# Kernel tuning notes

Hardware: AMD Instinct MI355X
Metric: run time of the kernel (lower is better)

## Reference

```python
import jax, jax.numpy as jnp
import numpy as np

HEADS = 4
KNN = 32
N_KEYS = 512
K_DIM = 512
HALF = K_DIM // 2
V_DIM = 1024
IN_DIM = 1024


def setup_inputs() -> dict:
    key = jax.random.key(0)
    k1, k2, k3, k4, k5 = jax.random.split(key, 5)
    x = jax.random.normal(k1, (1, 2048, IN_DIM), dtype=jnp.float32)
    w_q = jax.random.normal(k2, (HEADS * K_DIM, IN_DIM), dtype=jnp.float32) * (IN_DIM ** -0.5)
    b_q = jax.random.normal(k3, (HEADS * K_DIM,), dtype=jnp.float32) * 0.01
    # subkeys: uniform(-1/sqrt(half), 1/sqrt(half)) as in get_uniform_keys
    bound = 1.0 / np.sqrt(HALF)
    keys = jax.random.uniform(k4, (HEADS, 2, N_KEYS, HALF), dtype=jnp.float32,
                              minval=-bound, maxval=bound)
    # values: normal(0, v_dim**-0.5)
    values = jax.random.normal(k5, (N_KEYS * N_KEYS, V_DIM), dtype=jnp.float32) * (V_DIM ** -0.5)
    return {"x": x, "w_q": w_q, "b_q": b_q, "keys": keys, "values": values}


def reference(x, w_q, b_q, keys, values):
    B, S, D = x.shape
    bs = B * S
    # query projection: (bs, heads*k_dim) -> (bs, heads, 2, half)
    q = (x.reshape(bs, D) @ w_q.T + b_q).reshape(bs, HEADS, 2, HALF)
    # per-head, per-half subkey scores: (bs, heads, 2, n_keys)
    scores = jnp.einsum('bhtd,htnd->bhtn', q, keys)
    s_top, i_top = jax.lax.top_k(scores, KNN)          # (bs, heads, 2, knn)
    s1, s2 = s_top[:, :, 0], s_top[:, :, 1]
    i1, i2 = i_top[:, :, 0], i_top[:, :, 1]
    # cross-product of the two half top-k sets: (bs, heads, knn*knn)
    all_s = (s1[..., :, None] + s2[..., None, :]).reshape(bs, HEADS, KNN * KNN)
    all_i = (i1[..., :, None] * N_KEYS + i2[..., None, :]).reshape(bs, HEADS, KNN * KNN)
    best_s, best_pos = jax.lax.top_k(all_s, KNN)       # (bs, heads, knn)
    idx = jnp.take_along_axis(all_i, best_pos, axis=-1)
    # softmax over knn per head (matches softmax on scores.view(-1, knn))
    w = jax.nn.softmax(best_s, axis=-1).reshape(bs, HEADS * KNN)
    idx = idx.reshape(bs, HEADS * KNN)
    # weighted EmbeddingBag gather-sum over the value table
    out = jnp.einsum('bk,bkd->bd', w, values[idx])     # (bs, v_dim)
    return out.reshape(B, S, V_DIM)
```

## Files before the change

### kernel.cpp

```cpp
#include <hip/hip_runtime.h>
#include <math.h>

#define BSZ   2048
#define INDIM 1024
#define QDIM  2048
#define NHT   8
#define NKEYS 512
#define HALFD 256
#define KNN   32
#define VDIM  1024
#define HEADS 4

typedef _Float16 v8h __attribute__((ext_vector_type(8)));
typedef _Float16 v4h __attribute__((ext_vector_type(4)));
typedef float    v4f __attribute__((ext_vector_type(4)));

template<int KSHIFT, bool ASIDE>
__device__ __forceinline__ void split4(const float* __restrict__ in,
                                       _Float16* __restrict__ out, int i) {
  const long e0 = (long)i * 4;
  const int K = 1 << KSHIFT;
  const long r = e0 >> KSHIFT;
  const int k = (int)(e0 & (K - 1));
  const float4 a = *(const float4*)&in[e0];
  const float av[4] = {a.x, a.y, a.z, a.w};
  v4h hv, dv, mv;
  #pragma unroll
  for (int u = 0; u < 4; ++u) {
    const _Float16 hh = (_Float16)av[u];
    hv[u] = hh;
    mv[u] = (_Float16)((av[u] - (float)hh) * 64.0f);
    dv[u] = (_Float16)((float)hh * 0.015625f);
  }
  _Float16* base = out + r * (3L * K) + k;
  *(v4h*)(base)         = hv;
  *(v4h*)(base + K)     = ASIDE ? dv : mv;
  *(v4h*)(base + 2 * K) = ASIDE ? mv : dv;
}

__global__ __launch_bounds__(256) void split_all_kernel(
    const float* __restrict__ x, const float* __restrict__ wq, const float* __restrict__ ky,
    _Float16* __restrict__ xs, _Float16* __restrict__ wqs, _Float16* __restrict__ kys) {
  const int i = blockIdx.x * 256 + threadIdx.x;
  if (i < 524288)            split4<10, true >(x,  xs,  i);
  else if (i < 1048576)      split4<10, false>(wq, wqs, i - 524288);
  else                       split4<8,  false>(ky, kys, i - 1048576);
}

__device__ __forceinline__ void gload16(const _Float16* g, _Float16* l) {
  __builtin_amdgcn_global_load_lds(
      (const __attribute__((address_space(1))) unsigned int*)g,
      (__attribute__((address_space(3))) unsigned int*)l, 16, 0, 0);
}

#define WAITV8 asm volatile("s_waitcnt vmcnt(8)" ::: "memory")
#define WAITV4 asm volatile("s_waitcnt vmcnt(4)" ::: "memory")
#define WAITV0 asm volatile("s_waitcnt vmcnt(0)" ::: "memory")

template<bool Q_EPI>
__global__ __launch_bounds__(256) void mfma_gemm(
    const _Float16* __restrict__ A, int lda, long aBS,
    const _Float16* __restrict__ B, int ldb, long bBS,
    const float* __restrict__ bias,
    float* __restrict__ Cf, int ldc, long cBS,
    _Float16* __restrict__ Cq, int K) {
  __shared__ __align__(16) char smem[65536];
  _Float16* sh = (_Float16*)smem;
  const int t = threadIdx.x;
  const int z = blockIdx.z;
  const _Float16* Ab = A + (size_t)z * aBS;
  const _Float16* Bb = B + (size_t)z * bBS;
  const int m0 = blockIdx.y * 128, n0 = blockIdx.x * 128;

  const int o0 = t * 16;
  const int os = o0 ^ (((o0 >> 7) & 3) << 4);
  const int sr = os >> 6;
  const int sk = (os & 63) >> 1;
  const _Float16* gA0 = Ab + (size_t)(m0 + sr) * lda + sk;
  const _Float16* gA1 = Ab + (size_t)(m0 + sr + 64) * lda + sk;
  const _Float16* gB0 = Bb + (size_t)(n0 + sr) * ldb + sk;
  const _Float16* gB1 = Bb + (size_t)(n0 + sr + 64) * ldb + sk;
  const int t8 = t * 8;

  const int lane = t & 63, w = t >> 6;
  const int wr = (w >> 1) * 64, wc = (w & 1) * 64;
  const int fr = lane & 15, kg = lane >> 4;

  int aoff[4], boff[4];
  #pragma unroll
  for (int i = 0; i < 4; ++i) {
    const int ra = wr + i * 16 + fr;
    aoff[i] = (ra * 64 + ((kg ^ ((ra >> 1) & 3)) * 16)) >> 1;
    const int rb = wc + i * 16 + fr;
    boff[i] = ((rb * 64 + ((kg ^ ((rb >> 1) & 3)) * 16)) >> 1) + 4096;
  }

  v4f acc[4][4];
  #pragma unroll
  for (int i = 0; i < 4; ++i)
    #pragma unroll
    for (int j = 0; j < 4; ++j)
      acc[i][j] = (v4f){0.f, 0.f, 0.f, 0.f};

  const int nt = K >> 5;

  #pragma unroll
  for (int p = 0; p < 3; ++p) {
    _Float16* bb = sh + p * 8192;
    const size_t ko = (size_t)p * 32;
    gload16(gA0 + ko, bb + t8);
    gload16(gA1 + ko, bb + 2048 + t8);
    gload16(gB0 + ko, bb + 4096 + t8);
    gload16(gB1 + ko, bb + 6144 + t8);
  }
  WAITV8;
  __builtin_amdgcn_s_barrier();
  __builtin_amdgcn_sched_barrier(0);

  for (int tt = 0; tt < nt; ++tt) {
    const _Float16* bb = sh + (tt & 3) * 8192;
    if (tt + 3 < nt) {
      _Float16* nb = sh + ((tt + 3) & 3) * 8192;
      const size_t ko = (size_t)(tt + 3) * 32;
      gload16(gA0 + ko, nb + t8);
      gload16(gA1 + ko, nb + 2048 + t8);
      gload16(gB0 + ko, nb + 4096 + t8);
      gload16(gB1 + ko, nb + 6144 + t8);
    }
    v8h af[4], bf[4];
    #pragma unroll
    for (int i = 0; i < 4; ++i) af[i] = *(const v8h*)(bb + aoff[i]);
    #pragma unroll
    for (int j = 0; j < 4; ++j) bf[j] = *(const v8h*)(bb + boff[j]);
    #pragma unroll
    for (int i = 0; i < 4; ++i)
      #pragma unroll
      for (int j = 0; j < 4; ++j)
        acc[i][j] = __builtin_amdgcn_mfma_f32_16x16x32_f16(af[i], bf[j], acc[i][j], 0, 0, 0);
    if (tt + 3 < nt)      { WAITV8; }
    else if (tt + 2 < nt) { WAITV4; }
    else if (tt + 1 < nt) { WAITV0; }
    __builtin_amdgcn_s_barrier();
    __builtin_amdgcn_sched_barrier(0);
  }

  if (Q_EPI) {
    float* Ct = (float*)smem;
    #pragma unroll
    for (int half = 0; half < 2; ++half) {
      __syncthreads();
      if ((w & 1) == half) {
        #pragma unroll
        for (int j = 0; j < 4; ++j) {
          const int colq = j * 16 + fr;
          const float bv = bias[n0 + half * 64 + colq];
          #pragma unroll
          for (int i = 0; i < 4; ++i)
            #pragma unroll
            for (int rr = 0; rr < 4; ++rr)
              Ct[(wr + i * 16 + kg * 4 + rr) * 68 + colq] = acc[i][j][rr] + bv;
        }
      }
      __syncthreads();
      const int r = t >> 1, cb = (t & 1) * 32;
      const int gcol = n0 + half * 64 + cb;
      const int ht = gcol >> 8, dd = gcol & 255;
      _Float16* p = Cq + (size_t)(m0 + r) * (3 * HALFD * NHT) + ht * (3 * HALFD) + dd;
      #pragma unroll
      for (int u = 0; u < 32; u += 8) {
        float vv[8];
        *(float4*)&vv[0] = *(const float4*)&Ct[r * 68 + cb + u];
        *(float4*)&vv[4] = *(const float4*)&Ct[r * 68 + cb + u + 4];
        v8h hv, dv, mv;
        #pragma unroll
        for (int e = 0; e < 8; ++e) {
          const _Float16 hh = (_Float16)vv[e];
          hv[e] = hh;
          mv[e] = (_Float16)((vv[e] - (float)hh) * 64.0f);
          dv[e] = (_Float16)((float)hh * 0.015625f);
        }
        *(v8h*)(p + u) = hv;
        *(v8h*)(p + HALFD + u) = dv;
        *(v8h*)(p + 2 * HALFD + u) = mv;
      }
    }
  } else {
    float* Cb = Cf + (size_t)z * cBS;
    #pragma unroll
    for (int i = 0; i < 4; ++i)
      #pragma unroll
      for (int j = 0; j < 4; ++j)
        #pragma unroll
        for (int rr = 0; rr < 4; ++rr) {
          const int rowg = m0 + wr + i * 16 + kg * 4 + rr;
          const int colg = n0 + wc + j * 16 + fr;
          Cb[(size_t)rowg * ldc + colg] = acc[i][j][rr];
        }
  }
}

__global__ __launch_bounds__(256) void topk_all_gather_kernel(
    const float* __restrict__ S, const float* __restrict__ values,
    float* __restrict__ out) {
  __shared__ float ls1[4][32], ls2[4][32], sels[4][32];
  __shared__ int   li1[4][32], li2[4][32], seli[4][32];
  __shared__ float lw[128];
  __shared__ int   lidx[128];
  const int b = blockIdx.x, t = threadIdx.x;
  const int lane = t & 63, h = t >> 6;
  const float* srA = S + ((size_t)b * NHT + 2 * h) * NKEYS;
  const float* srB = srA + NKEYS;
  float va[8], vb[8];
  #pragma unroll
  for (int j = 0; j < 8; ++j) va[j] = srA[j * 64 + lane];
  #pragma unroll
  for (int j = 0; j < 8; ++j) vb[j] = srB[j * 64 + lane];

  for (int r = 0; r < KNN; ++r) {
    float bv = -INFINITY; int bi = 0x7fffffff;
    #pragma unroll
    for (int j = 0; j < 8; ++j) {
      const int idx = j * 64 + lane;
      if (va[j] > bv) { bv = va[j]; bi = idx; }
    }
    #pragma unroll
    for (int off = 32; off > 0; off >>= 1) {
      const float ov = __shfl_xor(bv, off);
      const int oi = __shfl_xor(bi, off);
      if (ov > bv || (ov == bv && oi < bi)) { bv = ov; bi = oi; }
    }
    if (lane == 0) { ls1[h][r] = bv; li1[h][r] = bi; }
    const int jj = bi >> 6;
    const bool mine = (bi & 63) == lane;
    #pragma unroll
    for (int j = 0; j < 8; ++j)
      if (mine && j == jj) va[j] = -INFINITY;
  }
  for (int r = 0; r < KNN; ++r) {
    float bv = -INFINITY; int bi = 0x7fffffff;
    #pragma unroll
    for (int j = 0; j < 8; ++j) {
      const int idx = j * 64 + lane;
      if (vb[j] > bv) { bv = vb[j]; bi = idx; }
    }
    #pragma unroll
    for (int off = 32; off > 0; off >>= 1) {
      const float ov = __shfl_xor(bv, off);
      const int oi = __shfl_xor(bi, off);
      if (ov > bv || (ov == bv && oi < bi)) { bv = ov; bi = oi; }
    }
    if (lane == 0) { ls2[h][r] = bv; li2[h][r] = bi; }
    const int jj = bi >> 6;
    const bool mine = (bi & 63) == lane;
    #pragma unroll
    for (int j = 0; j < 8; ++j)
      if (mine && j == jj) vb[j] = -INFINITY;
  }

  float v[16];
  #pragma unroll
  for (int c = 0; c < 16; ++c) {
    const int p = c * 64 + lane;
    v[c] = ls1[h][p >> 5] + ls2[h][p & 31];
  }
  for (int r = 0; r < KNN; ++r) {
    float bv = -INFINITY; int bp = 0x7fffffff;
    #pragma unroll
    for (int c = 0; c < 16; ++c) {
      const int p = c * 64 + lane;
      if (v[c] > bv) { bv = v[c]; bp = p; }
    }
    #pragma unroll
    for (int off = 32; off > 0; off >>= 1) {
      const float ov = __shfl_xor(bv, off);
      const int op = __shfl_xor(bp, off);
      if (ov > bv || (ov == bv && op < bp)) { bv = ov; bp = op; }
    }
    if (lane == 0) {
      sels[h][r] = bv;
      seli[h][r] = li1[h][bp >> 5] * NKEYS + li2[h][bp & 31];
    }
    const int cc = bp >> 6;
    const bool mine = (bp & 63) == lane;
    #pragma unroll
    for (int c = 0; c < 16; ++c)
      if (mine && c == cc) v[c] = -INFINITY;
  }
  const float m = sels[h][0];
  const float e = (lane < 32) ? expf(sels[h][lane] - m) : 0.0f;
  float s = e;
  #pragma unroll
  for (int off = 32; off > 0; off >>= 1) s += __shfl_xor(s, off);
  if (lane < 32) {
    lw[h * 32 + lane] = e / s;
    lidx[h * 32 + lane] = seli[h][lane];
  }
  __syncthreads();
  const int d0 = t * 4;
  float4 acc = {0.f, 0.f, 0.f, 0.f};
  #pragma unroll 8
  for (int k = 0; k < 128; ++k) {
    const float4 vv = *(const float4*)&values[(size_t)lidx[k] * VDIM + d0];
    const float ww = lw[k];
    acc.x = fmaf(ww, vv.x, acc.x);
    acc.y = fmaf(ww, vv.y, acc.y);
    acc.z = fmaf(ww, vv.z, acc.z);
    acc.w = fmaf(ww, vv.w, acc.w);
  }
  *(float4*)&out[(size_t)b * VDIM + d0] = acc;
}

extern "C" void kernel_launch(void* const* d_in, const int* in_sizes, int n_in,
                              void* d_out, int out_size, void* d_ws, size_t ws_size,
                              hipStream_t stream) {
  const float* x      = (const float*)d_in[0];
  const float* w_q    = (const float*)d_in[1];
  const float* b_q    = (const float*)d_in[2];
  const float* keys   = (const float*)d_in[3];
  const float* values = (const float*)d_in[4];
  float* out = (float*)d_out;

  char* ws = (char*)d_ws;
  _Float16* xs    = (_Float16*)(ws);
  _Float16* wqs   = (_Float16*)(ws + (16u  << 20));
  _Float16* keyss = (_Float16*)(ws + (32u  << 20));
  _Float16* Qs    = (_Float16*)(ws + (40u  << 20));
  float*    S     = (float*)   (ws + (68u  << 20));

  split_all_kernel<<<5120, 256, 0, stream>>>(x, w_q, keys, xs, wqs, keyss);

  mfma_gemm<true><<<dim3(QDIM / 128, BSZ / 128, 1), 256, 0, stream>>>(
      xs, 3 * INDIM, 0, wqs, 3 * INDIM, 0, b_q,
      nullptr, 0, 0, Qs, 3 * INDIM);
  mfma_gemm<false><<<dim3(NKEYS / 128, BSZ / 128, NHT), 256, 0, stream>>>(
      Qs, 3 * HALFD * NHT, 3 * HALFD, keyss, 3 * HALFD, (long)NKEYS * 3 * HALFD, nullptr,
      S, NHT * NKEYS, NKEYS, nullptr, 3 * HALFD);

  topk_all_gather_kernel<<<BSZ, 256, 0, stream>>>(S, values, out);
}
```

Baseline: 333.7 us.

## Deepen GEMM1 K-tile and overlap value gathers with top-k selection

The first projection GEMM becomes a dedicated kernel with a 64-wide K tile, a 4-stage LDS ring using 128KB of shared memory, and an 8-way XOR swizzle. Fewer, larger loop iterations are meant to cut barrier and issue overhead. The top-k/gather kernel now fetches each selected value row right after it is chosen and accumulates an online-softmax weighted sum per head, with a one-step software prefetch. A shared-memory reduction across the four heads replaces the separate 128-row gather loop, hiding gather latency behind selection. The cost is higher LDS use per block in GEMM1, which limits occupancy, and a changed floating-point summation order.

```diff
diff --git a/kernel.cpp b/kernel.cpp
--- a/kernel.cpp
+++ b/kernel.cpp
@@ -53,17 +53,145 @@
       (__attribute__((address_space(3))) unsigned int*)l, 16, 0, 0);
 }
 
-#define WAITV8 asm volatile("s_waitcnt vmcnt(8)" ::: "memory")
-#define WAITV4 asm volatile("s_waitcnt vmcnt(4)" ::: "memory")
-#define WAITV0 asm volatile("s_waitcnt vmcnt(0)" ::: "memory")
-
-template<bool Q_EPI>
-__global__ __launch_bounds__(256) void mfma_gemm(
+#define WAITV16 asm volatile("s_waitcnt vmcnt(16)" ::: "memory")
+#define WAITV8  asm volatile("s_waitcnt vmcnt(8)" ::: "memory")
+#define WAITV4  asm volatile("s_waitcnt vmcnt(4)" ::: "memory")
+#define WAITV0  asm volatile("s_waitcnt vmcnt(0)" ::: "memory")
+
+__global__ __launch_bounds__(256) void gemm1_kernel(
+    const _Float16* __restrict__ A, const _Float16* __restrict__ B,
+    const float* __restrict__ bias, _Float16* __restrict__ Cq) {
+  __shared__ __align__(16) char smem[131072];
+  _Float16* sh = (_Float16*)smem;
+  const int t = threadIdx.x;
+  const int m0 = blockIdx.y * 128, n0 = blockIdx.x * 128;
+  const int lane = t & 63, w = t >> 6;
+  const int wr = (w >> 1) * 64, wc = (w & 1) * 64;
+  const int fr = lane & 15, kg = lane >> 4;
+
+  const _Float16* gA[4]; const _Float16* gB[4];
+  int dA[4], dB[4];
+  #pragma unroll
+  for (int p = 0; p < 4; ++p) {
+    const int O = p * 4096 + t * 16;
+    const int os = O ^ (((O >> 7) & 7) << 4);
+    const int srow = os >> 7, sk = (os & 127) >> 1;
+    gA[p] = A + (size_t)(m0 + srow) * 3072 + sk;
+    gB[p] = B + (size_t)(n0 + srow) * 3072 + sk;
+    dA[p] = O >> 1;
+    dB[p] = (16384 + O) >> 1;
+  }
+
+  int aof[2][4], bof[2][4];
+  #pragma unroll
+  for (int ks = 0; ks < 2; ++ks)
+    #pragma unroll
+    for (int i = 0; i < 4; ++i) {
+      const int ra = wr + i * 16 + fr;
+      aof[ks][i] = (ra * 128 + ((((ks << 2) | kg) ^ (fr & 7)) << 4)) >> 1;
+      const int rb = wc + i * 16 + fr;
+      bof[ks][i] = ((rb * 128 + ((((ks << 2) | kg) ^ (fr & 7)) << 4)) >> 1) + 8192;
+    }
+
+  v4f acc[4][4];
+  #pragma unroll
+  for (int i = 0; i < 4; ++i)
+    #pragma unroll
+    for (int j = 0; j < 4; ++j)
+      acc[i][j] = (v4f){0.f, 0.f, 0.f, 0.f};
+
+  const int nt = 48;
+
+  #pragma unroll
+  for (int p2 = 0; p2 < 3; ++p2) {
+    _Float16* bb = sh + p2 * 16384;
+    const size_t ko = (size_t)p2 * 64;
+    #pragma unroll
+    for (int p = 0; p < 4; ++p) {
+      gload16(gA[p] + ko, bb + dA[p]);
+      gload16(gB[p] + ko, bb + dB[p]);
+    }
+  }
+  WAITV16;
+  __builtin_amdgcn_s_barrier();
+  __builtin_amdgcn_sched_barrier(0);
+
+  for (int tt = 0; tt < nt; ++tt) {
+    const _Float16* bb = sh + (tt & 3) * 16384;
+    if (tt + 3 < nt) {
+      _Float16* nb = sh + ((tt + 3) & 3) * 16384;
+      const size_t ko = (size_t)(tt + 3) * 64;
+      #pragma unroll
+      for (int p = 0; p < 4; ++p) {
+        gload16(gA[p] + ko, nb + dA[p]);
+        gload16(gB[p] + ko, nb + dB[p]);
+      }
+    }
+    #pragma unroll
+    for (int ks = 0; ks < 2; ++ks) {
+      v8h af[4], bf[4];
+      #pragma unroll
+      for (int i = 0; i < 4; ++i) af[i] = *(const v8h*)(bb + aof[ks][i]);
+      #pragma unroll
+      for (int j = 0; j < 4; ++j) bf[j] = *(const v8h*)(bb + bof[ks][j]);
+      #pragma unroll
+      for (int i = 0; i < 4; ++i)
+        #pragma unroll
+        for (int j = 0; j < 4; ++j)
+          acc[i][j] = __builtin_amdgcn_mfma_f32_16x16x32_f16(af[i], bf[j], acc[i][j], 0, 0, 0);
+    }
+    if (tt + 3 < nt)      { WAITV16; }
+    else if (tt + 2 < nt) { WAITV8; }
+    else if (tt + 1 < nt) { WAITV0; }
+    __builtin_amdgcn_s_barrier();
+    __builtin_amdgcn_sched_barrier(0);
+  }
+
+  float* Ct = (float*)smem;
+  #pragma unroll
+  for (int half = 0; half < 2; ++half) {
+    __syncthreads();
+    if ((w & 1) == half) {
+      #pragma unroll
+      for (int j = 0; j < 4; ++j) {
+        const int colq = j * 16 + fr;
+        const float bv = bias[n0 + half * 64 + colq];
+        #pragma unroll
+        for (int i = 0; i < 4; ++i)
+          #pragma unroll
+          for (int rr = 0; rr < 4; ++rr)
+            Ct[(wr + i * 16 + kg * 4 + rr) * 68 + colq] = acc[i][j][rr] + bv;
+      }
+    }
+    __syncthreads();
+    const int r = t >> 1, cb = (t & 1) * 32;
+    const int gcol = n0 + half * 64 + cb;
+    const int ht = gcol >> 8, dd = gcol & 255;
+    _Float16* p = Cq + (size_t)(m0 + r) * (3 * HALFD * NHT) + ht * (3 * HALFD) + dd;
+    #pragma unroll
+    for (int u = 0; u < 32; u += 8) {
+      float vv[8];
+      *(float4*)&vv[0] = *(const float4*)&Ct[r * 68 + cb + u];
+      *(float4*)&vv[4] = *(const float4*)&Ct[r * 68 + cb + u + 4];
+      v8h hv, dv, mv;
+      #pragma unroll
+      for (int e = 0; e < 8; ++e) {
+        const _Float16 hh = (_Float16)vv[e];
+        hv[e] = hh;
+        mv[e] = (_Float16)((vv[e] - (float)hh) * 64.0f);
+        dv[e] = (_Float16)((float)hh * 0.015625f);
+      }
+      *(v8h*)(p + u) = hv;
+      *(v8h*)(p + HALFD + u) = dv;
+      *(v8h*)(p + 2 * HALFD + u) = mv;
+    }
+  }
+}
+
+__global__ __launch_bounds__(256) void gemm2_kernel(
     const _Float16* __restrict__ A, int lda, long aBS,
     const _Float16* __restrict__ B, int ldb, long bBS,
-    const float* __restrict__ bias,
-    float* __restrict__ Cf, int ldc, long cBS,
-    _Float16* __restrict__ Cq, int K) {
+    float* __restrict__ Cf, int ldc, long cBS, int K) {
   __shared__ __align__(16) char smem[65536];
   _Float16* sh = (_Float16*)smem;
   const int t = threadIdx.x;
@@ -144,68 +272,25 @@
     __builtin_amdgcn_sched_barrier(0);
   }
 
-  if (Q_EPI) {
-    float* Ct = (float*)smem;
-    #pragma unroll
-    for (int half = 0; half < 2; ++half) {
-      __syncthreads();
-      if ((w & 1) == half) {
-        #pragma unroll
-        for (int j = 0; j < 4; ++j) {
-          const int colq = j * 16 + fr;
-          const float bv = bias[n0 + half * 64 + colq];
-          #pragma unroll
-          for (int i = 0; i < 4; ++i)
-            #pragma unroll
-            for (int rr = 0; rr < 4; ++rr)
-              Ct[(wr + i * 16 + kg * 4 + rr) * 68 + colq] = acc[i][j][rr] + bv;
-        }
+  float* Cb = Cf + (size_t)z * cBS;
+  #pragma unroll
+  for (int i = 0; i < 4; ++i)
+    #pragma unroll
+    for (int j = 0; j < 4; ++j)
+      #pragma unroll
+      for (int rr = 0; rr < 4; ++rr) {
+        const int rowg = m0 + wr + i * 16 + kg * 4 + rr;
+        const int colg = n0 + wc + j * 16 + fr;
+        Cb[(size_t)rowg * ldc + colg] = acc[i][j][rr];
       }
-      __syncthreads();
-      const int r = t >> 1, cb = (t & 1) * 32;
-      const int gcol = n0 + half * 64 + cb;
-      const int ht = gcol >> 8, dd = gcol & 255;
-      _Float16* p = Cq + (size_t)(m0 + r) * (3 * HALFD * NHT) + ht * (3 * HALFD) + dd;
-      #pragma unroll
-      for (int u = 0; u < 32; u += 8) {
-        float vv[8];
-        *(float4*)&vv[0] = *(const float4*)&Ct[r * 68 + cb + u];
-        *(float4*)&vv[4] = *(const float4*)&Ct[r * 68 + cb + u + 4];
-        v8h hv, dv, mv;
-        #pragma unroll
-        for (int e = 0; e < 8; ++e) {
-          const _Float16 hh = (_Float16)vv[e];
-          hv[e] = hh;
-          mv[e] = (_Float16)((vv[e] - (float)hh) * 64.0f);
-          dv[e] = (_Float16)((float)hh * 0.015625f);
-        }
-        *(v8h*)(p + u) = hv;
-        *(v8h*)(p + HALFD + u) = dv;
-        *(v8h*)(p + 2 * HALFD + u) = mv;
-      }
-    }
-  } else {
-    float* Cb = Cf + (size_t)z * cBS;
-    #pragma unroll
-    for (int i = 0; i < 4; ++i)
-      #pragma unroll
-      for (int j = 0; j < 4; ++j)
-        #pragma unroll
-        for (int rr = 0; rr < 4; ++rr) {
-          const int rowg = m0 + wr + i * 16 + kg * 4 + rr;
-          const int colg = n0 + wc + j * 16 + fr;
-          Cb[(size_t)rowg * ldc + colg] = acc[i][j][rr];
-        }
-  }
 }
 
 __global__ __launch_bounds__(256) void topk_all_gather_kernel(
     const float* __restrict__ S, const float* __restrict__ values,
     float* __restrict__ out) {
-  __shared__ float ls1[4][32], ls2[4][32], sels[4][32];
-  __shared__ int   li1[4][32], li2[4][32], seli[4][32];
-  __shared__ float lw[128];
-  __shared__ int   lidx[128];
+  __shared__ float ls1[4][32], ls2[4][32];
+  __shared__ int   li1[4][32], li2[4][32];
+  __shared__ float red[4][1024];
   const int b = blockIdx.x, t = threadIdx.x;
   const int lane = t & 63, h = t >> 6;
   const float* srA = S + ((size_t)b * NHT + 2 * h) * NKEYS;
@@ -263,6 +348,9 @@
     const int p = c * 64 + lane;
     v[c] = ls1[h][p >> 5] + ls2[h][p & 31];
   }
+  float4 acc0 = {0,0,0,0}, acc1 = {0,0,0,0}, acc2 = {0,0,0,0}, acc3 = {0,0,0,0};
+  float4 pv0, pv1, pv2, pv3;
+  float pe = 0.0f, m = 0.0f, Z = 0.0f;
   for (int r = 0; r < KNN; ++r) {
     float bv = -INFINITY; int bp = 0x7fffffff;
     #pragma unroll
@@ -276,38 +364,56 @@
       const int op = __shfl_xor(bp, off);
       if (ov > bv || (ov == bv && op < bp)) { bv = ov; bp = op; }
     }
-    if (lane == 0) {
-      sels[h][r] = bv;
-      seli[h][r] = li1[h][bp >> 5] * NKEYS + li2[h][bp & 31];
-    }
+    const int row = li1[h][bp >> 5] * NKEYS + li2[h][bp & 31];
+    if (r == 0) m = bv;
+    const float e = expf(bv - m);
+    Z += e;
+    const float4* vp = (const float4*)(values + (size_t)row * VDIM) + lane;
+    const float4 c0 = vp[0], c1 = vp[64], c2 = vp[128], c3 = vp[192];
+    if (r > 0) {
+      acc0.x = fmaf(pe, pv0.x, acc0.x); acc0.y = fmaf(pe, pv0.y, acc0.y);
+      acc0.z = fmaf(pe, pv0.z, acc0.z); acc0.w = fmaf(pe, pv0.w, acc0.w);
+      acc1.x = fmaf(pe, pv1.x, acc1.x); acc1.y = fmaf(pe, pv1.y, acc1.y);
+      acc1.z = fmaf(pe, pv1.z, acc1.z); acc1.w = fmaf(pe, pv1.w, acc1.w);
+      acc2.x = fmaf(pe, pv2.x, acc2.x); acc2.y = fmaf(pe, pv2.y, acc2.y);
+      acc2.z = fmaf(pe, pv2.z, acc2.z); acc2.w = fmaf(pe, pv2.w, acc2.w);
+      acc3.x = fmaf(pe, pv3.x, acc3.x); acc3.y = fmaf(pe, pv3.y, acc3.y);
+      acc3.z = fmaf(pe, pv3.z, acc3.z); acc3.w = fmaf(pe, pv3.w, acc3.w);
+    }
+    pv0 = c0; pv1 = c1; pv2 = c2; pv3 = c3; pe = e;
     const int cc = bp >> 6;
     const bool mine = (bp & 63) == lane;
     #pragma unroll
     for (int c = 0; c < 16; ++c)
       if (mine && c == cc) v[c] = -INFINITY;
   }
-  const float m = sels[h][0];
-  const float e = (lane < 32) ? expf(sels[h][lane] - m) : 0.0f;
-  float s = e;
-  #pragma unroll
-  for (int off = 32; off > 0; off >>= 1) s += __shfl_xor(s, off);
-  if (lane < 32) {
-    lw[h * 32 + lane] = e / s;
-    lidx[h * 32 + lane] = seli[h][lane];
-  }
+  const float invZ = 1.0f / Z;
+  acc0.x = fmaf(pe, pv0.x, acc0.x); acc0.y = fmaf(pe, pv0.y, acc0.y);
+  acc0.z = fmaf(pe, pv0.z, acc0.z); acc0.w = fmaf(pe, pv0.w, acc0.w);
+  acc1.x = fmaf(pe, pv1.x, acc1.x); acc1.y = fmaf(pe, pv1.y, acc1.y);
+  acc1.z = fmaf(pe, pv1.z, acc1.z); acc1.w = fmaf(pe, pv1.w, acc1.w);
+  acc2.x = fmaf(pe, pv2.x, acc2.x); acc2.y = fmaf(pe, pv2.y, acc2.y);
+  acc2.z = fmaf(pe, pv2.z, acc2.z); acc2.w = fmaf(pe, pv2.w, acc2.w);
+  acc3.x = fmaf(pe, pv3.x, acc3.x); acc3.y = fmaf(pe, pv3.y, acc3.y);
+  acc3.z = fmaf(pe, pv3.z, acc3.z); acc3.w = fmaf(pe, pv3.w, acc3.w);
+  acc0.x *= invZ; acc0.y *= invZ; acc0.z *= invZ; acc0.w *= invZ;
+  acc1.x *= invZ; acc1.y *= invZ; acc1.z *= invZ; acc1.w *= invZ;
+  acc2.x *= invZ; acc2.y *= invZ; acc2.z *= invZ; acc2.w *= invZ;
+  acc3.x *= invZ; acc3.y *= invZ; acc3.z *= invZ; acc3.w *= invZ;
+
+  float4* rp = (float4*)&red[h][0];
+  rp[lane] = acc0; rp[lane + 64] = acc1; rp[lane + 128] = acc2; rp[lane + 192] = acc3;
   __syncthreads();
-  const int d0 = t * 4;
-  float4 acc = {0.f, 0.f, 0.f, 0.f};
-  #pragma unroll 8
-  for (int k = 0; k < 128; ++k) {
-    const float4 vv = *(const float4*)&values[(size_t)lidx[k] * VDIM + d0];
-    const float ww = lw[k];
-    acc.x = fmaf(ww, vv.x, acc.x);
-    acc.y = fmaf(ww, vv.y, acc.y);
-    acc.z = fmaf(ww, vv.z, acc.z);
-    acc.w = fmaf(ww, vv.w, acc.w);
-  }
-  *(float4*)&out[(size_t)b * VDIM + d0] = acc;
+  const float4* r0 = (const float4*)&red[0][0];
+  const float4* r1 = (const float4*)&red[1][0];
+  const float4* r2 = (const float4*)&red[2][0];
+  const float4* r3 = (const float4*)&red[3][0];
+  float4 o;
+  o.x = r0[t].x + r1[t].x + r2[t].x + r3[t].x;
+  o.y = r0[t].y + r1[t].y + r2[t].y + r3[t].y;
+  o.z = r0[t].z + r1[t].z + r2[t].z + r3[t].z;
+  o.w = r0[t].w + r1[t].w + r2[t].w + r3[t].w;
+  ((float4*)&out[(size_t)b * VDIM])[t] = o;
 }
 
 extern "C" void kernel_launch(void* const* d_in, const int* in_sizes, int n_in,
@@ -329,12 +435,10 @@
 
   split_all_kernel<<<5120, 256, 0, stream>>>(x, w_q, keys, xs, wqs, keyss);
 
-  mfma_gemm<true><<<dim3(QDIM / 128, BSZ / 128, 1), 256, 0, stream>>>(
-      xs, 3 * INDIM, 0, wqs, 3 * INDIM, 0, b_q,
-      nullptr, 0, 0, Qs, 3 * INDIM);
-  mfma_gemm<false><<<dim3(NKEYS / 128, BSZ / 128, NHT), 256, 0, stream>>>(
-      Qs, 3 * HALFD * NHT, 3 * HALFD, keyss, 3 * HALFD, (long)NKEYS * 3 * HALFD, nullptr,
-      S, NHT * NKEYS, NKEYS, nullptr, 3 * HALFD);
+  gemm1_kernel<<<dim3(QDIM / 128, BSZ / 128), 256, 0, stream>>>(xs, wqs, b_q, Qs);
+  gemm2_kernel<<<dim3(NKEYS / 128, BSZ / 128, NHT), 256, 0, stream>>>(
+      Qs, 3 * HALFD * NHT, 3 * HALFD, keyss, 3 * HALFD, (long)NKEYS * 3 * HALFD,
+      S, NHT * NKEYS, NKEYS, 3 * HALFD);
 
   topk_all_gather_kernel<<<BSZ, 256, 0, stream>>>(S, values, out);
 }
```

Result: no change. 333.8 us (+0.0%).

## Interleave value-row gathers with per-head top-k selection loop

Applied to the files above, without the earlier changes.

Each head's wavefront now fetches the selected value row as soon as each top-k winner is found, accumulating with an unnormalized online softmax weight and a one-step software pipeline. Previously the gather ran only after all selections were done. The aim is to hide gather memory latency behind the serial selection rounds. A 16KB shared buffer then sums the four heads' partial results. This costs extra registers and LDS and may lower occupancy.

```diff
diff --git a/kernel.cpp b/kernel.cpp
--- a/kernel.cpp
+++ b/kernel.cpp
@@ -202,10 +202,9 @@
 __global__ __launch_bounds__(256) void topk_all_gather_kernel(
     const float* __restrict__ S, const float* __restrict__ values,
     float* __restrict__ out) {
-  __shared__ float ls1[4][32], ls2[4][32], sels[4][32];
-  __shared__ int   li1[4][32], li2[4][32], seli[4][32];
-  __shared__ float lw[128];
-  __shared__ int   lidx[128];
+  __shared__ float ls1[4][32], ls2[4][32];
+  __shared__ int   li1[4][32], li2[4][32];
+  __shared__ float red[4][1024];
   const int b = blockIdx.x, t = threadIdx.x;
   const int lane = t & 63, h = t >> 6;
   const float* srA = S + ((size_t)b * NHT + 2 * h) * NKEYS;
@@ -263,6 +262,9 @@
     const int p = c * 64 + lane;
     v[c] = ls1[h][p >> 5] + ls2[h][p & 31];
   }
+  float4 acc0 = {0,0,0,0}, acc1 = {0,0,0,0}, acc2 = {0,0,0,0}, acc3 = {0,0,0,0};
+  float4 pv0, pv1, pv2, pv3;
+  float pe = 0.0f, m = 0.0f, Z = 0.0f;
   for (int r = 0; r < KNN; ++r) {
     float bv = -INFINITY; int bp = 0x7fffffff;
     #pragma unroll
@@ -276,38 +278,56 @@
       const int op = __shfl_xor(bp, off);
       if (ov > bv || (ov == bv && op < bp)) { bv = ov; bp = op; }
     }
-    if (lane == 0) {
-      sels[h][r] = bv;
-      seli[h][r] = li1[h][bp >> 5] * NKEYS + li2[h][bp & 31];
-    }
+    const int row = li1[h][bp >> 5] * NKEYS + li2[h][bp & 31];
+    if (r == 0) m = bv;
+    const float e = expf(bv - m);
+    Z += e;
+    const float4* vp = (const float4*)(values + (size_t)row * VDIM) + lane;
+    const float4 c0 = vp[0], c1 = vp[64], c2 = vp[128], c3 = vp[192];
+    if (r > 0) {
+      acc0.x = fmaf(pe, pv0.x, acc0.x); acc0.y = fmaf(pe, pv0.y, acc0.y);
+      acc0.z = fmaf(pe, pv0.z, acc0.z); acc0.w = fmaf(pe, pv0.w, acc0.w);
+      acc1.x = fmaf(pe, pv1.x, acc1.x); acc1.y = fmaf(pe, pv1.y, acc1.y);
+      acc1.z = fmaf(pe, pv1.z, acc1.z); acc1.w = fmaf(pe, pv1.w, acc1.w);
+      acc2.x = fmaf(pe, pv2.x, acc2.x); acc2.y = fmaf(pe, pv2.y, acc2.y);
+      acc2.z = fmaf(pe, pv2.z, acc2.z); acc2.w = fmaf(pe, pv2.w, acc2.w);
+      acc3.x = fmaf(pe, pv3.x, acc3.x); acc3.y = fmaf(pe, pv3.y, acc3.y);
+      acc3.z = fmaf(pe, pv3.z, acc3.z); acc3.w = fmaf(pe, pv3.w, acc3.w);
+    }
+    pv0 = c0; pv1 = c1; pv2 = c2; pv3 = c3; pe = e;
     const int cc = bp >> 6;
     const bool mine = (bp & 63) == lane;
     #pragma unroll
     for (int c = 0; c < 16; ++c)
       if (mine && c == cc) v[c] = -INFINITY;
   }
-  const float m = sels[h][0];
-  const float e = (lane < 32) ? expf(sels[h][lane] - m) : 0.0f;
-  float s = e;
-  #pragma unroll
-  for (int off = 32; off > 0; off >>= 1) s += __shfl_xor(s, off);
-  if (lane < 32) {
-    lw[h * 32 + lane] = e / s;
-    lidx[h * 32 + lane] = seli[h][lane];
-  }
+  const float invZ = 1.0f / Z;
+  acc0.x = fmaf(pe, pv0.x, acc0.x); acc0.y = fmaf(pe, pv0.y, acc0.y);
+  acc0.z = fmaf(pe, pv0.z, acc0.z); acc0.w = fmaf(pe, pv0.w, acc0.w);
+  acc1.x = fmaf(pe, pv1.x, acc1.x); acc1.y = fmaf(pe, pv1.y, acc1.y);
+  acc1.z = fmaf(pe, pv1.z, acc1.z); acc1.w = fmaf(pe, pv1.w, acc1.w);
+  acc2.x = fmaf(pe, pv2.x, acc2.x); acc2.y = fmaf(pe, pv2.y, acc2.y);
+  acc2.z = fmaf(pe, pv2.z, acc2.z); acc2.w = fmaf(pe, pv2.w, acc2.w);
+  acc3.x = fmaf(pe, pv3.x, acc3.x); acc3.y = fmaf(pe, pv3.y, acc3.y);
+  acc3.z = fmaf(pe, pv3.z, acc3.z); acc3.w = fmaf(pe, pv3.w, acc3.w);
+  acc0.x *= invZ; acc0.y *= invZ; acc0.z *= invZ; acc0.w *= invZ;
+  acc1.x *= invZ; acc1.y *= invZ; acc1.z *= invZ; acc1.w *= invZ;
+  acc2.x *= invZ; acc2.y *= invZ; acc2.z *= invZ; acc2.w *= invZ;
+  acc3.x *= invZ; acc3.y *= invZ; acc3.z *= invZ; acc3.w *= invZ;
+
+  float4* rp = (float4*)&red[h][0];
+  rp[lane] = acc0; rp[lane + 64] = acc1; rp[lane + 128] = acc2; rp[lane + 192] = acc3;
   __syncthreads();
-  const int d0 = t * 4;
-  float4 acc = {0.f, 0.f, 0.f, 0.f};
-  #pragma unroll 8
-  for (int k = 0; k < 128; ++k) {
-    const float4 vv = *(const float4*)&values[(size_t)lidx[k] * VDIM + d0];
-    const float ww = lw[k];
-    acc.x = fmaf(ww, vv.x, acc.x);
-    acc.y = fmaf(ww, vv.y, acc.y);
-    acc.z = fmaf(ww, vv.z, acc.z);
-    acc.w = fmaf(ww, vv.w, acc.w);
-  }
-  *(float4*)&out[(size_t)b * VDIM + d0] = acc;
+  const float4* r0 = (const float4*)&red[0][0];
+  const float4* r1 = (const float4*)&red[1][0];
+  const float4* r2 = (const float4*)&red[2][0];
+  const float4* r3 = (const float4*)&red[3][0];
+  float4 o;
+  o.x = r0[t].x + r1[t].x + r2[t].x + r3[t].x;
+  o.y = r0[t].y + r1[t].y + r2[t].y + r3[t].y;
+  o.z = r0[t].z + r1[t].z + r2[t].z + r3[t].z;
+  o.w = r0[t].w + r1[t].w + r2[t].w + r3[t].w;
+  ((float4*)&out[(size_t)b * VDIM])[t] = o;
 }
 
 extern "C" void kernel_launch(void* const* d_in, const int* in_sizes, int n_in,
```

Measured after the change: 336.9 us. About the same (+1.0%).
